# Kernel tuning notes

Measured on AMD Instinct MI355X. Metric: run time of the kernel, lower is better.

Reference implementation:

```python
import jax, jax.numpy as jnp
import numpy as np

B, C, H, W = 2, 256, 48, 48
NH = 4          # heads (and SE ratio)
DK = C // NH    # 64


def conv1x1(x, w, b):
    # x: [B,Cin,H,W], w: [Cout,Cin], b: [Cout]
    return jnp.einsum('oc,bchw->bohw', w, x) + b[None, :, None, None]


def rtrans(q_in, k_in, v_in, qw, qb, kw, kb, vw, vb):
    b, c, h_, w_ = q_in.shape
    n = h_ * w_
    q = conv1x1(q_in, qw, qb).reshape(b, NH, DK, n).transpose(0, 1, 3, 2)  # [B,h,N,dk]
    k = conv1x1(k_in, kw, kb).reshape(b, NH, DK, n)                         # [B,h,dk,N]
    v = conv1x1(v_in, vw, vb).reshape(b, NH, DK, n)                         # [B,h,dk,N]
    scores = jnp.einsum('bhnd,bhdm->bhnm', q, k) / jnp.sqrt(jnp.asarray(DK, q.dtype))
    attn = jax.nn.softmax(scores, axis=-1)                                  # [B,h,N,N]
    out = jnp.einsum('bhdn,bhnm->bhdm', v, attn)                            # [B,h,dk,N]
    return out.reshape(b, c, h_, w_)


def setup_inputs() -> dict:
    key = jax.random.key(0)
    ks = jax.random.split(key, 16)
    s = 0.02
    d = {
        'x': jax.random.normal(ks[0], (B, C, H, W), jnp.float32),
        'y': jax.random.normal(ks[1], (B, C, H, W), jnp.float32),
        # RScaling: fc1 Conv2d(2C, C//ratio, 1), fc2 Conv2d(C//ratio, 2C, 1); ratio=NH
        'sc_fc1_w': jax.random.normal(ks[2], (C // NH, 2 * C), jnp.float32) * s,
        'sc_fc1_b': jnp.zeros((C // NH,), jnp.float32),
        'sc_fc2_w': jax.random.normal(ks[3], (2 * C, C // NH), jnp.float32) * s,
        'sc_fc2_b': jnp.zeros((2 * C,), jnp.float32),
        # RTrans 1
        't1_qw': jax.random.normal(ks[4], (C, C), jnp.float32) * s,
        't1_qb': jnp.zeros((C,), jnp.float32),
        't1_kw': jax.random.normal(ks[5], (C, C), jnp.float32) * s,
        't1_kb': jnp.zeros((C,), jnp.float32),
        't1_vw': jax.random.normal(ks[6], (C, C), jnp.float32) * s,
        't1_vb': jnp.zeros((C,), jnp.float32),
        # RTrans 2 (ST=True)
        't2_qw': jax.random.normal(ks[7], (C, C), jnp.float32) * s,
        't2_qb': jnp.zeros((C,), jnp.float32),
        't2_kw': jax.random.normal(ks[8], (C, C), jnp.float32) * s,
        't2_kb': jnp.zeros((C,), jnp.float32),
        't2_vw': jax.random.normal(ks[9], (C, C), jnp.float32) * s,
        't2_vb': jnp.zeros((C,), jnp.float32),
        # RGating: Conv2d(2C, 2, 1)
        'gate_w': jax.random.normal(ks[10], (2, 2 * C), jnp.float32) * s,
        'gate_b': jnp.zeros((2,), jnp.float32),
    }
    return d


def reference(x, y, sc_fc1_w, sc_fc1_b, sc_fc2_w, sc_fc2_b,
              t1_qw, t1_qb, t1_kw, t1_kb, t1_vw, t1_vb,
              t2_qw, t2_qb, t2_kw, t2_kb, t2_vw, t2_vb,
              gate_w, gate_b):
    c = x.shape[1]
    # --- RScaling (SE squeeze-excite on concatenated streams) ---
    cat = jnp.concatenate([x, y], axis=1)                       # [B,2C,H,W]
    pooled = cat.mean(axis=(2, 3), keepdims=True)               # [B,2C,1,1]
    f = conv1x1(jax.nn.relu(conv1x1(pooled, sc_fc1_w, sc_fc1_b)), sc_fc2_w, sc_fc2_b)
    g = jax.nn.sigmoid(f)                                       # [B,2C,1,1]
    x = x * g[:, :c] + x
    y = y * g[:, c:] + y
    # --- RTrans 1: x = attn(q=x, k=y, v=y) ---
    x = rtrans(x, y, y, t1_qw, t1_qb, t1_kw, t1_kb, t1_vw, t1_vb)
    # --- RTrans 2 (ST): y = attn(q=y, k=x_new, v=x_new) ---
    y = rtrans(y, x, x, t2_qw, t2_qb, t2_kw, t2_kb, t2_vw, t2_vb)
    # --- RGating ---
    gate = jax.nn.sigmoid(conv1x1(jnp.concatenate([x, y], axis=1), gate_w, gate_b))  # [B,2,H,W]
    x = x * gate[:, :1] + x
    y = y * gate[:, 1:] + y
    return (x, y)
```

## Files before the change

kernel.cpp:

```cpp
#include <hip/hip_runtime.h>
#include <hip/hip_bf16.h>
#include <math.h>

typedef __hip_bfloat16 bf16;
typedef unsigned short u16;
typedef __attribute__((ext_vector_type(8))) short short8;
typedef __attribute__((ext_vector_type(4))) float f32x4;

#define BB  2
#define CC  256
#define NHH 4
#define DKK 64
#define NN  2304
#define NT  36
#define NT2 18
#define MS  4
#define NTM 9
#define WSTR 88
#define MFMA16(a,b,c) __builtin_amdgcn_mfma_f32_16x16x32_bf16(a, b, c, 0, 0, 0)

__device__ __forceinline__ float u2f(u16 u){ return __uint_as_float(((unsigned)u) << 16); }
__device__ __forceinline__ u16 f2u(float f){
    unsigned u = __float_as_uint(f);
    unsigned r = u + 0x7FFFu + ((u >> 16) & 1u);
    return (u16)(r >> 16);
}

__device__ __forceinline__ float ldv(const void* p, size_t i, int bf){
    return bf ? u2f(((const u16*)p)[i]) : ((const float*)p)[i];
}
__device__ __forceinline__ void stv(void* p, size_t i, float v, int bf){
    if (bf) ((u16*)p)[i] = f2u(v);
    else    ((float*)p)[i] = v;
}
__device__ __forceinline__ short8 ldw8(const void* p, size_t i, int bf){
    if (bf) return *(const short8*)((const u16*)p + i);
    const float* f = (const float*)p + i;
    short8 r;
    #pragma unroll
    for (int k = 0; k < 8; k++) r[k] = (short)f2u(f[k]);
    return r;
}

__global__ void detect_kernel(const void* __restrict__ x, int* __restrict__ flg){
    const u16* u = (const u16*)x;
    int t = threadIdx.x;
    bool ok = true;
    for (int i = 0; i < 8; i++){
        u16 v = u[t*8 + i];
        int e = (v >> 7) & 0xFF;
        ok = ok && (((v & 0x7FFF) == 0) || (e >= 96 && e <= 143));
    }
    unsigned long long b = __ballot(ok);
    if (t == 0) *flg = (b == 0xFFFFFFFFFFFFFFFFull) ? 1 : 0;
}

__global__ void pool_kernel(const void* __restrict__ x, const void* __restrict__ y,
                            const int* __restrict__ flg, float* __restrict__ pooled){
    int bf = *flg;
    int bid = blockIdx.x;
    int b = bid >> 9, cc = bid & 511;
    const void* src = (cc < CC) ? x : y;
    size_t base = ((size_t)b*CC + (cc & 255))*NN;
    float s = 0.f;
    for (int i = threadIdx.x; i < NN; i += 256) s += ldv(src, base + i, bf);
    __shared__ float red[4];
    for (int off = 32; off; off >>= 1) s += __shfl_down(s, off, 64);
    if ((threadIdx.x & 63) == 0) red[threadIdx.x >> 6] = s;
    __syncthreads();
    if (threadIdx.x == 0)
        pooled[bid] = (red[0]+red[1]+red[2]+red[3]) * (1.0f/(float)NN);
}

__global__ void se_fc1_kernel(const float* __restrict__ pooled,
                              const void* __restrict__ w1, const void* __restrict__ b1,
                              const int* __restrict__ flg, float* __restrict__ f1){
    int bf = *flg;
    int bid = blockIdx.x;
    int b = bid >> 6, f = bid & 63;
    int lane = threadIdx.x;
    const float* ps = pooled + b*512;
    float a = 0.f;
    #pragma unroll
    for (int k = 0; k < 8; k++){
        int c = lane*8 + k;
        a += ldv(w1, (size_t)f*512 + c, bf) * ps[c];
    }
    #pragma unroll
    for (int off = 32; off; off >>= 1) a += __shfl_down(a, off, 64);
    if (lane == 0)
        f1[b*64 + f] = fmaxf(a + ldv(b1, f, bf), 0.f);
}

__launch_bounds__(512)
__global__ void se_fc2_kernel(const float* __restrict__ f1,
                              const void* __restrict__ w2, const void* __restrict__ b2v,
                              const int* __restrict__ flg, float* __restrict__ gse){
    int bf = *flg;
    int b = blockIdx.x;
    int o = threadIdx.x;
    __shared__ float f1s[64];
    if (o < 64) f1s[o] = f1[b*64 + o];
    __syncthreads();
    float a = ldv(b2v, o, bf);
    #pragma unroll
    for (int j = 0; j < 64; j++) a += ldv(w2, (size_t)o*64 + j, bf) * f1s[j];
    gse[b*512 + o] = 1.f + 1.f/(1.f + __expf(-a));
}

__global__ void transpose2_kernel(const void* __restrict__ x, const void* __restrict__ y,
                                  const float* __restrict__ gse, const int* __restrict__ flg,
                                  u16* __restrict__ xsT, u16* __restrict__ ysT){
    int bf = *flg;
    int z = blockIdx.z;
    int b = z >> 1, which = z & 1;
    const void* src = which ? y : x;
    const float* gs = gse + b*512 + (which ? 256 : 0);
    u16* dst = which ? ysT : xsT;
    int ct = blockIdx.y, nt = blockIdx.x;
    int t = threadIdx.x;
    int nl = t & 63, cq = t >> 6;
    #pragma unroll
    for (int i = 0; i < 16; i++){
        int c = ct*64 + cq*16 + i;
        float v = ldv(src, ((size_t)b*CC + c)*NN + nt*64 + nl, bf) * gs[c];
        dst[((size_t)b*NN + nt*64 + nl)*CC + c] = f2u(v);
    }
}

__launch_bounds__(256)
__global__ void conv3_mfma(const u16* __restrict__ Xq, const u16* __restrict__ Xkv,
                           const void* __restrict__ wq, const void* __restrict__ bq,
                           const void* __restrict__ wk, const void* __restrict__ bk,
                           const void* __restrict__ wv, const void* __restrict__ bv_,
                           const int* __restrict__ flg,
                           u16* __restrict__ QT, u16* __restrict__ KT, u16* __restrict__ Vb){
    int bf = *flg;
    int bhD = blockIdx.x & 7;
    int q = blockIdx.x >> 3;
    int op = q / 36, nt = q % 36;
    int b = bhD >> 2, ot = bhD & 3;
    const u16* X = (op == 0) ? Xq : Xkv;
    const void* W    = (op == 0) ? wq : (op == 1) ? wk : wv;
    const void* bias = (op == 0) ? bq : (op == 1) ? bk : bv_;
    u16* Y = (op == 0) ? QT : (op == 1) ? KT : Vb;
    int transT = (op < 2);
    float oscale = (op == 1) ? 0.125f : 1.0f;
    int lane = threadIdx.x & 63, wv_ = threadIdx.x >> 6;
    int c15 = lane & 15, quad = lane >> 4;
    const u16* Xb = X + ((size_t)b*NN + nt*64)*CC;
    int oa = ot*64 + wv_*16 + c15;
    f32x4 zf = {0.f,0.f,0.f,0.f};
    f32x4 acc[4] = {zf,zf,zf,zf};
    #pragma unroll
    for (int kc = 0; kc < CC; kc += 32){
        short8 aw = ldw8(W, (size_t)oa*CC + kc + quad*8, bf);
        #pragma unroll
        for (int j = 0; j < 4; j++){
            short8 bx = *(const short8*)(Xb + (size_t)(j*16 + c15)*CC + kc + quad*8);
            acc[j] = MFMA16(aw, bx, acc[j]);
        }
    }
    int od = ot*64 + wv_*16 + quad*4;
    float bvr[4];
    #pragma unroll
    for (int r = 0; r < 4; r++) bvr[r] = ldv(bias, od + r, bf);
    #pragma unroll
    for (int j = 0; j < 4; j++){
        int n = nt*64 + j*16 + c15;
        #pragma unroll
        for (int r = 0; r < 4; r++){
            int o = od + r;
            float val = (acc[j][r] + bvr[r]) * oscale;
            size_t idx = transT
              ? (((size_t)(b*NHH + (o >> 6))*NN + n)*DKK + (o & 63))
              : (((size_t)b*CC + o)*NN + n);
            Y[idx] = f2u(val);
        }
    }
}

__launch_bounds__(256)
__global__ void attn_stats_mfma(const u16* __restrict__ QT, const u16* __restrict__ KT,
                                float* __restrict__ gL){
    int bh = blockIdx.x & 7;
    int r2 = blockIdx.x >> 3;
    int ntile = r2 % 36, ms = r2 / 36;
    int lane = threadIdx.x & 63, wv = threadIdx.x >> 6;
    int c15 = lane & 15, quad = lane >> 4;
    const u16* Qb = QT + (size_t)bh*NN*DKK;
    const u16* Kb = KT + (size_t)bh*NN*DKK;
    size_t qo = (size_t)(ntile*64 + wv*16 + c15)*DKK + quad*8;
    short8 a0 = *(const short8*)(Qb + qo);
    short8 a1 = *(const short8*)(Qb + qo + 32);
    float ll[4] = {0.f,0.f,0.f,0.f};
    f32x4 z = {0.f,0.f,0.f,0.f};
    for (int it = 0; it < NTM; it++){
        int mt = ms*NTM + it;
        f32x4 s[4];
        #pragma unroll
        for (int j = 0; j < 4; j++){
            size_t ko = (size_t)(mt*64 + j*16 + c15)*DKK + quad*8;
            short8 b0 = *(const short8*)(Kb + ko);
            short8 b1 = *(const short8*)(Kb + ko + 32);
            f32x4 t = MFMA16(a0, b0, z);
            s[j]     = MFMA16(a1, b1, t);
        }
        #pragma unroll
        for (int r = 0; r < 4; r++)
            ll[r] += __expf(s[0][r]) + __expf(s[1][r]) + __expf(s[2][r]) + __expf(s[3][r]);
    }
    #pragma unroll
    for (int d = 1; d < 16; d <<= 1)
        #pragma unroll
        for (int r = 0; r < 4; r++)
            ll[r] += __shfl_xor(ll[r], d, 16);
    if (c15 == 0){
        #pragma unroll
        for (int r = 0; r < 4; r++){
            int n = ntile*64 + wv*16 + quad*4 + r;
            gL[((size_t)ms*BB*NHH + bh)*NN + n] = ll[r];
        }
    }
}

__global__ void stats_combine(const float* __restrict__ gL, float* __restrict__ Li){
    int idx = blockIdx.x*256 + threadIdx.x;
    if (idx >= BB*NHH*NN) return;
    float ll = 0.f;
    #pragma unroll
    for (int ms = 0; ms < MS; ms++)
        ll += gL[(size_t)ms*BB*NHH*NN + idx];
    Li[idx] = 1.f/ll;
}

__launch_bounds__(512)
__global__ void attn_out_mfma(const u16* __restrict__ QT, const u16* __restrict__ KT,
                              const u16* __restrict__ V, const float* __restrict__ Li,
                              const int* __restrict__ flg,
                              void* __restrict__ O, size_t ooff, u16* __restrict__ OT){
    int bf = *flg;
    int bh = blockIdx.x & 7;
    int mtile = blockIdx.x >> 3;
    int tid = threadIdx.x;
    int lane = tid & 63, wv5 = tid >> 6;
    int g = wv5 >> 2, wv = wv5 & 3;
    int c15 = lane & 15, quad = lane >> 4;
    const u16* Qb = QT + (size_t)bh*NN*DKK;
    const u16* Kb = KT + (size_t)bh*NN*DKK;
    const u16* Vb = V + (size_t)bh*DKK*NN;
    const float* Lp = Li + (size_t)bh*NN;
    __shared__ __align__(16) u16 wT[2][2][32][WSTR];
    __shared__ __align__(16) float osum[64][34];
    short8 kb0[2], kb1[2];
    #pragma unroll
    for (int j = 0; j < 2; j++){
        size_t ko = (size_t)(mtile*32 + j*16 + c15)*DKK + quad*8;
        kb0[j] = *(const short8*)(Kb + ko);
        kb1[j] = *(const short8*)(Kb + ko + 32);
    }
    f32x4 z = {0.f,0.f,0.f,0.f};
    f32x4 o4[2] = {z,z};
    int nt0 = g*NT2;
    size_t qo0 = (size_t)(nt0*64 + wv*16 + c15)*DKK + quad*8;
    short8 a0 = *(const short8*)(Qb + qo0);
    short8 a1 = *(const short8*)(Qb + qo0 + 32);
    size_t vo0 = (size_t)(wv*16 + c15)*NN + nt0*64 + quad*8;
    short8 av0 = *(const short8*)(Vb + vo0);
    short8 av1 = *(const short8*)(Vb + vo0 + 32);
    for (int it = 0; it < NT2; it++){
        int nt = g*NT2 + it;
        int p = it & 1;
        f32x4 s[2];
        #pragma unroll
        for (int j = 0; j < 2; j++){
            f32x4 t = MFMA16(a0, kb0[j], z);
            s[j]    = MFMA16(a1, kb1[j], t);
        }
        short8 a0n = a0, a1n = a1, av0n = av0, av1n = av1;
        if (it + 1 < NT2){
            size_t qn = (size_t)((nt+1)*64 + wv*16 + c15)*DKK + quad*8;
            a0n = *(const short8*)(Qb + qn);
            a1n = *(const short8*)(Qb + qn + 32);
            size_t vn = (size_t)(wv*16 + c15)*NN + (nt+1)*64 + quad*8;
            av0n = *(const short8*)(Vb + vn);
            av1n = *(const short8*)(Vb + vn + 32);
        }
        int nb = nt*64 + wv*16 + quad*4;
        float iL[4];
        #pragma unroll
        for (int r = 0; r < 4; r++) iL[r] = Lp[nb+r];
        #pragma unroll
        for (int j = 0; j < 2; j++){
            ushort4 pk;
            pk.x = f2u(__expf(s[j][0]) * iL[0]);
            pk.y = f2u(__expf(s[j][1]) * iL[1]);
            pk.z = f2u(__expf(s[j][2]) * iL[2]);
            pk.w = f2u(__expf(s[j][3]) * iL[3]);
            *(ushort4*)&wT[g][p][j*16 + c15][wv*16 + quad*4] = pk;
        }
        __syncthreads();
        #pragma unroll
        for (int j = 0; j < 2; j++){
            short8 b0 = *(const short8*)&wT[g][p][j*16 + c15][quad*8];
            short8 b1 = *(const short8*)&wT[g][p][j*16 + c15][32 + quad*8];
            o4[j] = MFMA16(av0, b0, o4[j]);
            o4[j] = MFMA16(av1, b1, o4[j]);
        }
        a0 = a0n; a1 = a1n; av0 = av0n; av1 = av1n;
    }
    if (g == 1){
        #pragma unroll
        for (int j = 0; j < 2; j++)
            #pragma unroll
            for (int r = 0; r < 4; r++)
                osum[wv*16 + quad*4 + r][j*16 + c15] = o4[j][r];
    }
    __syncthreads();
    if (g == 0){
        int brow = bh >> 2, head = bh & 3;
        #pragma unroll
        for (int j = 0; j < 2; j++){
            int m = mtile*32 + j*16 + c15;
            #pragma unroll
            for (int r = 0; r < 4; r++){
                int d = wv*16 + quad*4 + r;
                float val = o4[j][r] + osum[d][j*16 + c15];
                stv(O, ooff + ((size_t)brow*CC + head*DKK + d)*NN + m, val, bf);
                if (OT) OT[((size_t)brow*NN + m)*CC + head*DKK + d] = f2u(val);
            }
        }
    }
}

__global__ void gate_part_kernel(const void* __restrict__ out, const void* __restrict__ gw,
                                 const int* __restrict__ flg, float* __restrict__ gpart){
    int bf = *flg;
    const size_t SZ = (size_t)BB*CC*NN;
    int b = blockIdx.z, g = blockIdx.y;
    int nb = blockIdx.x*64;
    int t = threadIdx.x;
    int nl = t & 63, sub = t >> 6;
    __shared__ float r0[4][64], r1[4][64];
    float a0 = 0.f, a1 = 0.f;
    int cbase = g*128 + sub*32;
    for (int i = 0; i < 32; i++){
        int cc = cbase + i;
        size_t idx = (cc < 256 ? ((size_t)b*CC + cc)*NN
                               : SZ + ((size_t)b*CC + (cc-256))*NN) + nb + nl;
        float v = ldv(out, idx, bf);
        a0 += ldv(gw, cc, bf)*v;
        a1 += ldv(gw, 512 + cc, bf)*v;
    }
    r0[sub][nl] = a0; r1[sub][nl] = a1;
    __syncthreads();
    if (t < 64){
        float s0 = r0[0][t]+r0[1][t]+r0[2][t]+r0[3][t];
        float s1 = r1[0][t]+r1[1][t]+r1[2][t]+r1[3][t];
        int n = nb + t;
        gpart[(((size_t)b*4 + g)*2 + 0)*NN + n] = s0;
        gpart[(((size_t)b*4 + g)*2 + 1)*NN + n] = s1;
    }
}

__global__ void gate_combine_kernel(const float* __restrict__ gpart, const void* __restrict__ gb,
                                    const int* __restrict__ flg, float* __restrict__ gates){
    int bf = *flg;
    int idx = blockIdx.x*256 + threadIdx.x;
    if (idx >= BB*NN) return;
    int b = idx / NN, n = idx % NN;
    float s0 = ldv(gb, 0, bf), s1 = ldv(gb, 1, bf);
    #pragma unroll
    for (int g = 0; g < 4; g++){
        s0 += gpart[(((size_t)b*4 + g)*2 + 0)*NN + n];
        s1 += gpart[(((size_t)b*4 + g)*2 + 1)*NN + n];
    }
    gates[((size_t)b*2 + 0)*NN + n] = 1.f + 1.f/(1.f + __expf(-s0));
    gates[((size_t)b*2 + 1)*NN + n] = 1.f + 1.f/(1.f + __expf(-s1));
}

__global__ void rescale_kernel(const float* __restrict__ gates, const int* __restrict__ flg,
                               void* __restrict__ out){
    int bf = *flg;
    const size_t SZ = (size_t)BB*CC*NN;
    const size_t nq = (2*SZ) >> 2;
    for (size_t u = (size_t)blockIdx.x*256 + threadIdx.x; u < nq; u += (size_t)gridDim.x*256){
        size_t flat = u*4;
        int half = (int)(flat / SZ);
        size_t rem = flat % SZ;
        int b = (int)(rem / ((size_t)CC*NN));
        int n = (int)(rem % NN);
        const float* gp = gates + ((size_t)b*2 + half)*NN + n;
        #pragma unroll
        for (int k = 0; k < 4; k++)
            stv(out, flat + k, ldv(out, flat + k, bf) * gp[k], bf);
    }
}

extern "C" void kernel_launch(void* const* d_in, const int* in_sizes, int n_in,
                              void* d_out, int out_size, void* d_ws, size_t ws_size,
                              hipStream_t stream){
    (void)in_sizes; (void)n_in; (void)out_size; (void)ws_size;
    const void* x    = d_in[0];
    const void* y    = d_in[1];
    const void* sc1w = d_in[2];
    const void* sc1b = d_in[3];
    const void* sc2w = d_in[4];
    const void* sc2b = d_in[5];
    const void *t1qw = d_in[6],  *t1qb = d_in[7];
    const void *t1kw = d_in[8],  *t1kb = d_in[9];
    const void *t1vw = d_in[10], *t1vb = d_in[11];
    const void *t2qw = d_in[12], *t2qb = d_in[13];
    const void *t2kw = d_in[14], *t2kb = d_in[15];
    const void *t2vw = d_in[16], *t2vb = d_in[17];
    const void *gw   = d_in[18], *gb   = d_in[19];

    const size_t SZ = (size_t)BB*CC*NN;
    const size_t BHN = (size_t)BB*NHH*NN;
    char* wsb = (char*)d_ws;
    int*   flg    = (int*)wsb;
    float* pooled = (float*)(wsb + 16);
    float* f1     = pooled + 1024;
    float* gse    = f1 + 128;
    float* Lb     = gse + 1024;
    float* gL     = Lb + BHN;
    float* gpart  = gL + MS*BHN;
    float* gates  = gpart + (size_t)BB*4*2*NN;
    u16* xsT = (u16*)(gates + (size_t)BB*2*NN);
    u16* ysT = xsT + SZ;
    u16* QT  = ysT + SZ;
    u16* KT  = QT + SZ;
    u16* Vb  = KT + SZ;

    dim3 tg2(NT, 4, BB*2);
    dim3 gg(NT, 4, BB);

    detect_kernel<<<1, 64, 0, stream>>>(x, flg);
    pool_kernel<<<1024, 256, 0, stream>>>(x, y, flg, pooled);
    se_fc1_kernel<<<BB*64, 64, 0, stream>>>(pooled, sc1w, sc1b, flg, f1);
    se_fc2_kernel<<<BB, 512, 0, stream>>>(f1, sc2w, sc2b, flg, gse);

    transpose2_kernel<<<tg2, 256, 0, stream>>>(x, y, gse, flg, xsT, ysT);

    conv3_mfma<<<864, 256, 0, stream>>>(xsT, ysT, t1qw, t1qb, t1kw, t1kb, t1vw, t1vb,
                                        flg, QT, KT, Vb);
    attn_stats_mfma<<<1152, 256, 0, stream>>>(QT, KT, gL);
    stats_combine<<<72, 256, 0, stream>>>(gL, Lb);
    attn_out_mfma<<<576, 512, 0, stream>>>(QT, KT, Vb, Lb, flg, d_out, 0, xsT);

    conv3_mfma<<<864, 256, 0, stream>>>(ysT, xsT, t2qw, t2qb, t2kw, t2kb, t2vw, t2vb,
                                        flg, QT, KT, Vb);
    attn_stats_mfma<<<1152, 256, 0, stream>>>(QT, KT, gL);
    stats_combine<<<72, 256, 0, stream>>>(gL, Lb);
    attn_out_mfma<<<576, 512, 0, stream>>>(QT, KT, Vb, Lb, flg, d_out, SZ, (u16*)nullptr);

    gate_part_kernel<<<gg, 256, 0, stream>>>(d_out, gw, flg, gpart);
    gate_combine_kernel<<<18, 256, 0, stream>>>(gpart, gb, flg, gates);
    rescale_kernel<<<1024, 256, 0, stream>>>(gates, flg, d_out);
}
```

Before: 428.1 us.

## Restructure attention output kernel with per-wave tiles and fuse stats and SE kernels

The attention-output kernel is reorganized. Each 256-thread block now owns 64 output columns (two 32-wide strips), and each wave computes a full 64-row Q tile by 32 columns with private LDS staging of P, which removes the block-wide __syncthreads in the inner loop. The stats_combine kernel is folded in: each block reduces the partial softmax denominators into LDS at startup. The two SE fc kernels are merged into one. The aims are fewer launches, less synchronization and more reuse of the K fragments, at the cost of more registers per wave, half as many blocks, and Q/V loads with no prefetch.

Measured after the change: 462.8 us. +8.1%, slower.

```diff
diff --git a/kernel.cpp b/kernel.cpp
--- a/kernel.cpp
+++ b/kernel.cpp
@@ -13,10 +13,8 @@
 #define DKK 64
 #define NN  2304
 #define NT  36
-#define NT2 18
 #define MS  4
 #define NTM 9
-#define WSTR 88
 #define MFMA16(a,b,c) __builtin_amdgcn_mfma_f32_16x16x32_bf16(a, b, c, 0, 0, 0)
 
 __device__ __forceinline__ float u2f(u16 u){ return __uint_as_float(((unsigned)u) << 16); }
@@ -72,40 +70,38 @@
         pooled[bid] = (red[0]+red[1]+red[2]+red[3]) * (1.0f/(float)NN);
 }
 
-__global__ void se_fc1_kernel(const float* __restrict__ pooled,
-                              const void* __restrict__ w1, const void* __restrict__ b1,
-                              const int* __restrict__ flg, float* __restrict__ f1){
-    int bf = *flg;
-    int bid = blockIdx.x;
-    int b = bid >> 6, f = bid & 63;
-    int lane = threadIdx.x;
-    const float* ps = pooled + b*512;
+__launch_bounds__(512)
+__global__ void se_kernel(const float* __restrict__ pooled,
+                          const void* __restrict__ w1, const void* __restrict__ b1,
+                          const void* __restrict__ w2, const void* __restrict__ b2v,
+                          const int* __restrict__ flg, float* __restrict__ gse){
+    int bf = *flg;
+    int b = blockIdx.x;
+    int t = threadIdx.x;
+    __shared__ float ps[512];
+    __shared__ float r1[64][9];
+    __shared__ float f1s[64];
+    ps[t] = pooled[b*512 + t];
+    __syncthreads();
+    int f = t >> 3, sub = t & 7;
     float a = 0.f;
-    #pragma unroll
-    for (int k = 0; k < 8; k++){
-        int c = lane*8 + k;
+    for (int i = 0; i < 64; i++){
+        int c = sub*64 + i;
         a += ldv(w1, (size_t)f*512 + c, bf) * ps[c];
     }
-    #pragma unroll
-    for (int off = 32; off; off >>= 1) a += __shfl_down(a, off, 64);
-    if (lane == 0)
-        f1[b*64 + f] = fmaxf(a + ldv(b1, f, bf), 0.f);
-}
-
-__launch_bounds__(512)
-__global__ void se_fc2_kernel(const float* __restrict__ f1,
-                              const void* __restrict__ w2, const void* __restrict__ b2v,
-                              const int* __restrict__ flg, float* __restrict__ gse){
-    int bf = *flg;
-    int b = blockIdx.x;
-    int o = threadIdx.x;
-    __shared__ float f1s[64];
-    if (o < 64) f1s[o] = f1[b*64 + o];
-    __syncthreads();
-    float a = ldv(b2v, o, bf);
-    #pragma unroll
-    for (int j = 0; j < 64; j++) a += ldv(w2, (size_t)o*64 + j, bf) * f1s[j];
-    gse[b*512 + o] = 1.f + 1.f/(1.f + __expf(-a));
+    r1[f][sub] = a;
+    __syncthreads();
+    if (t < 64){
+        float s = ldv(b1, t, bf);
+        #pragma unroll
+        for (int k = 0; k < 8; k++) s += r1[t][k];
+        f1s[t] = fmaxf(s, 0.f);
+    }
+    __syncthreads();
+    float a2 = ldv(b2v, t, bf);
+    #pragma unroll
+    for (int j = 0; j < 64; j++) a2 += ldv(w2, (size_t)t*64 + j, bf) * f1s[j];
+    gse[b*512 + t] = 1.f + 1.f/(1.f + __expf(-a2));
 }
 
 __global__ void transpose2_kernel(const void* __restrict__ x, const void* __restrict__ y,
@@ -224,112 +220,114 @@
     }
 }
 
-__global__ void stats_combine(const float* __restrict__ gL, float* __restrict__ Li){
-    int idx = blockIdx.x*256 + threadIdx.x;
-    if (idx >= BB*NHH*NN) return;
-    float ll = 0.f;
-    #pragma unroll
-    for (int ms = 0; ms < MS; ms++)
-        ll += gL[(size_t)ms*BB*NHH*NN + idx];
-    Li[idx] = 1.f/ll;
-}
-
-__launch_bounds__(512)
+__launch_bounds__(256, 2)
 __global__ void attn_out_mfma(const u16* __restrict__ QT, const u16* __restrict__ KT,
-                              const u16* __restrict__ V, const float* __restrict__ Li,
+                              const u16* __restrict__ V, const float* __restrict__ gL,
                               const int* __restrict__ flg,
                               void* __restrict__ O, size_t ooff, u16* __restrict__ OT){
     int bf = *flg;
     int bh = blockIdx.x & 7;
-    int mtile = blockIdx.x >> 3;
+    int mt = blockIdx.x >> 3;
     int tid = threadIdx.x;
-    int lane = tid & 63, wv5 = tid >> 6;
-    int g = wv5 >> 2, wv = wv5 & 3;
+    int lane = tid & 63, w = tid >> 6;
+    int strip = w & 1, half = w >> 1;
     int c15 = lane & 15, quad = lane >> 4;
+    int mbase = mt*64 + strip*32;
     const u16* Qb = QT + (size_t)bh*NN*DKK;
     const u16* Kb = KT + (size_t)bh*NN*DKK;
     const u16* Vb = V + (size_t)bh*DKK*NN;
-    const float* Lp = Li + (size_t)bh*NN;
-    __shared__ __align__(16) u16 wT[2][2][32][WSTR];
-    __shared__ __align__(16) float osum[64][34];
-    short8 kb0[2], kb1[2];
-    #pragma unroll
-    for (int j = 0; j < 2; j++){
-        size_t ko = (size_t)(mtile*32 + j*16 + c15)*DKK + quad*8;
-        kb0[j] = *(const short8*)(Kb + ko);
-        kb1[j] = *(const short8*)(Kb + ko + 32);
+
+    __shared__ __align__(16) float Lis[NN];
+    __shared__ __align__(16) u16 pT[4][32][72];
+    __shared__ __align__(16) float osum[2][64][33];
+
+    const size_t BHN = (size_t)BB*NHH*NN;
+    for (int i = tid; i < NN; i += 256){
+        size_t o = (size_t)bh*NN + i;
+        Lis[i] = 1.f / (gL[o] + gL[BHN + o] + gL[2*BHN + o] + gL[3*BHN + o]);
+    }
+    __syncthreads();
+
+    short8 kb[2][2];
+    #pragma unroll
+    for (int ms2 = 0; ms2 < 2; ms2++){
+        size_t ko = (size_t)(mbase + ms2*16 + c15)*DKK + quad*8;
+        kb[ms2][0] = *(const short8*)(Kb + ko);
+        kb[ms2][1] = *(const short8*)(Kb + ko + 32);
     }
     f32x4 z = {0.f,0.f,0.f,0.f};
-    f32x4 o4[2] = {z,z};
-    int nt0 = g*NT2;
-    size_t qo0 = (size_t)(nt0*64 + wv*16 + c15)*DKK + quad*8;
-    short8 a0 = *(const short8*)(Qb + qo0);
-    short8 a1 = *(const short8*)(Qb + qo0 + 32);
-    size_t vo0 = (size_t)(wv*16 + c15)*NN + nt0*64 + quad*8;
-    short8 av0 = *(const short8*)(Vb + vo0);
-    short8 av1 = *(const short8*)(Vb + vo0 + 32);
-    for (int it = 0; it < NT2; it++){
-        int nt = g*NT2 + it;
-        int p = it & 1;
-        f32x4 s[2];
-        #pragma unroll
-        for (int j = 0; j < 2; j++){
-            f32x4 t = MFMA16(a0, kb0[j], z);
-            s[j]    = MFMA16(a1, kb1[j], t);
-        }
-        short8 a0n = a0, a1n = a1, av0n = av0, av1n = av1;
-        if (it + 1 < NT2){
-            size_t qn = (size_t)((nt+1)*64 + wv*16 + c15)*DKK + quad*8;
-            a0n = *(const short8*)(Qb + qn);
-            a1n = *(const short8*)(Qb + qn + 32);
-            size_t vn = (size_t)(wv*16 + c15)*NN + (nt+1)*64 + quad*8;
-            av0n = *(const short8*)(Vb + vn);
-            av1n = *(const short8*)(Vb + vn + 32);
-        }
-        int nb = nt*64 + wv*16 + quad*4;
-        float iL[4];
-        #pragma unroll
-        for (int r = 0; r < 4; r++) iL[r] = Lp[nb+r];
-        #pragma unroll
-        for (int j = 0; j < 2; j++){
-            ushort4 pk;
-            pk.x = f2u(__expf(s[j][0]) * iL[0]);
-            pk.y = f2u(__expf(s[j][1]) * iL[1]);
-            pk.z = f2u(__expf(s[j][2]) * iL[2]);
-            pk.w = f2u(__expf(s[j][3]) * iL[3]);
-            *(ushort4*)&wT[g][p][j*16 + c15][wv*16 + quad*4] = pk;
-        }
-        __syncthreads();
-        #pragma unroll
-        for (int j = 0; j < 2; j++){
-            short8 b0 = *(const short8*)&wT[g][p][j*16 + c15][quad*8];
-            short8 b1 = *(const short8*)&wT[g][p][j*16 + c15][32 + quad*8];
-            o4[j] = MFMA16(av0, b0, o4[j]);
-            o4[j] = MFMA16(av1, b1, o4[j]);
-        }
-        a0 = a0n; a1 = a1n; av0 = av0n; av1 = av1n;
-    }
-    if (g == 1){
-        #pragma unroll
-        for (int j = 0; j < 2; j++)
+    f32x4 o4[4][2];
+    #pragma unroll
+    for (int dg = 0; dg < 4; dg++){ o4[dg][0] = z; o4[dg][1] = z; }
+
+    for (int it = 0; it < 18; it++){
+        int nt = half*18 + it;
+        const u16* Qn = Qb + (size_t)nt*64*DKK;
+        f32x4 s[4][2];
+        #pragma unroll
+        for (int g = 0; g < 4; g++){
+            short8 a0 = *(const short8*)(Qn + (size_t)(g*16 + c15)*DKK + quad*8);
+            short8 a1 = *(const short8*)(Qn + (size_t)(g*16 + c15)*DKK + quad*8 + 32);
             #pragma unroll
-            for (int r = 0; r < 4; r++)
-                osum[wv*16 + quad*4 + r][j*16 + c15] = o4[j][r];
-    }
-    __syncthreads();
-    if (g == 0){
+            for (int ms2 = 0; ms2 < 2; ms2++){
+                f32x4 t = MFMA16(a0, kb[ms2][0], z);
+                s[g][ms2] = MFMA16(a1, kb[ms2][1], t);
+            }
+        }
+        #pragma unroll
+        for (int g = 0; g < 4; g++){
+            float4 il = *(const float4*)&Lis[nt*64 + g*16 + quad*4];
+            #pragma unroll
+            for (int ms2 = 0; ms2 < 2; ms2++){
+                unsigned p01 = (unsigned)f2u(__expf(s[g][ms2][0])*il.x)
+                             | ((unsigned)f2u(__expf(s[g][ms2][1])*il.y) << 16);
+                unsigned p23 = (unsigned)f2u(__expf(s[g][ms2][2])*il.z)
+                             | ((unsigned)f2u(__expf(s[g][ms2][3])*il.w) << 16);
+                *(uint2*)&pT[w][ms2*16 + c15][g*16 + quad*4] = make_uint2(p01, p23);
+            }
+        }
+        short8 pb[2][2];
+        #pragma unroll
+        for (int ms2 = 0; ms2 < 2; ms2++){
+            pb[ms2][0] = *(const short8*)&pT[w][ms2*16 + c15][quad*8];
+            pb[ms2][1] = *(const short8*)&pT[w][ms2*16 + c15][32 + quad*8];
+        }
+        #pragma unroll
+        for (int dg = 0; dg < 4; dg++){
+            size_t vo = (size_t)(dg*16 + c15)*NN + nt*64 + quad*8;
+            short8 av0 = *(const short8*)(Vb + vo);
+            short8 av1 = *(const short8*)(Vb + vo + 32);
+            #pragma unroll
+            for (int ms2 = 0; ms2 < 2; ms2++){
+                o4[dg][ms2] = MFMA16(av0, pb[ms2][0], o4[dg][ms2]);
+                o4[dg][ms2] = MFMA16(av1, pb[ms2][1], o4[dg][ms2]);
+            }
+        }
+    }
+    if (half == 1){
+        #pragma unroll
+        for (int dg = 0; dg < 4; dg++)
+            #pragma unroll
+            for (int ms2 = 0; ms2 < 2; ms2++)
+                #pragma unroll
+                for (int r = 0; r < 4; r++)
+                    osum[strip][dg*16 + quad*4 + r][ms2*16 + c15] = o4[dg][ms2][r];
+    }
+    __syncthreads();
+    if (half == 0){
         int brow = bh >> 2, head = bh & 3;
         #pragma unroll
-        for (int j = 0; j < 2; j++){
-            int m = mtile*32 + j*16 + c15;
+        for (int dg = 0; dg < 4; dg++)
             #pragma unroll
-            for (int r = 0; r < 4; r++){
-                int d = wv*16 + quad*4 + r;
-                float val = o4[j][r] + osum[d][j*16 + c15];
-                stv(O, ooff + ((size_t)brow*CC + head*DKK + d)*NN + m, val, bf);
-                if (OT) OT[((size_t)brow*NN + m)*CC + head*DKK + d] = f2u(val);
-            }
-        }
+            for (int ms2 = 0; ms2 < 2; ms2++)
+                #pragma unroll
+                for (int r = 0; r < 4; r++){
+                    int d = dg*16 + quad*4 + r;
+                    int m = mbase + ms2*16 + c15;
+                    float val = o4[dg][ms2][r] + osum[strip][d][ms2*16 + c15];
+                    stv(O, ooff + ((size_t)brow*CC + head*DKK + d)*NN + m, val, bf);
+                    if (OT) OT[((size_t)brow*NN + m)*CC + head*DKK + d] = f2u(val);
+                }
     }
 }
 
@@ -420,10 +418,8 @@
     char* wsb = (char*)d_ws;
     int*   flg    = (int*)wsb;
     float* pooled = (float*)(wsb + 16);
-    float* f1     = pooled + 1024;
-    float* gse    = f1 + 128;
-    float* Lb     = gse + 1024;
-    float* gL     = Lb + BHN;
+    float* gse    = pooled + 1024;
+    float* gL     = gse + 1024;
     float* gpart  = gL + MS*BHN;
     float* gates  = gpart + (size_t)BB*4*2*NN;
     u16* xsT = (u16*)(gates + (size_t)BB*2*NN);
@@ -437,22 +433,19 @@
 
     detect_kernel<<<1, 64, 0, stream>>>(x, flg);
     pool_kernel<<<1024, 256, 0, stream>>>(x, y, flg, pooled);
-    se_fc1_kernel<<<BB*64, 64, 0, stream>>>(pooled, sc1w, sc1b, flg, f1);
-    se_fc2_kernel<<<BB, 512, 0, stream>>>(f1, sc2w, sc2b, flg, gse);
+    se_kernel<<<BB, 512, 0, stream>>>(pooled, sc1w, sc1b, sc2w, sc2b, flg, gse);
 
     transpose2_kernel<<<tg2, 256, 0, stream>>>(x, y, gse, flg, xsT, ysT);
 
     conv3_mfma<<<864, 256, 0, stream>>>(xsT, ysT, t1qw, t1qb, t1kw, t1kb, t1vw, t1vb,
                                         flg, QT, KT, Vb);
     attn_stats_mfma<<<1152, 256, 0, stream>>>(QT, KT, gL);
-    stats_combine<<<72, 256, 0, stream>>>(gL, Lb);
-    attn_out_mfma<<<576, 512, 0, stream>>>(QT, KT, Vb, Lb, flg, d_out, 0, xsT);
+    attn_out_mfma<<<288, 256, 0, stream>>>(QT, KT, Vb, gL, flg, d_out, 0, xsT);
 
     conv3_mfma<<<864, 256, 0, stream>>>(ysT, xsT, t2qw, t2qb, t2kw, t2kb, t2vw, t2vb,
                                         flg, QT, KT, Vb);
     attn_stats_mfma<<<1152, 256, 0, stream>>>(QT, KT, gL);
-    stats_combine<<<72, 256, 0, stream>>>(gL, Lb);
-    attn_out_mfma<<<576, 512, 0, stream>>>(QT, KT, Vb, Lb, flg, d_out, SZ, (u16*)nullptr);
+    attn_out_mfma<<<288, 256, 0, stream>>>(QT, KT, Vb, gL, flg, d_out, SZ, (u16*)nullptr);
 
     gate_part_kernel<<<gg, 256, 0, stream>>>(d_out, gw, flg, gpart);
     gate_combine_kernel<<<18, 256, 0, stream>>>(gpart, gb, flg, gates);
```
